# Kernel tuning notes

Hardware: AMD Instinct MI355X
Metric: run time of the kernel (lower is better)

## Reference

```python
import jax, jax.numpy as jnp
import numpy as np

N = 8192   # number of points (p) == number of reference points (r); must match for final bmm
D = 1024   # feature width of the Linear projections


def setup_inputs() -> dict:
    key = jax.random.key(0)
    ks = jax.random.split(key, 8)
    s = 1.0 / np.sqrt(D)
    return {
        "p": jax.random.normal(ks[0], (N, D), dtype=jnp.float32),
        "r": jax.random.normal(ks[1], (N, D), dtype=jnp.float32),
        "Wh": jax.random.uniform(ks[2], (D, D), jnp.float32, -s, s),
        "bh": jax.random.uniform(ks[3], (D,), jnp.float32, -s, s),
        "Wl": jax.random.uniform(ks[4], (D, D), jnp.float32, -s, s),
        "bl": jax.random.uniform(ks[5], (D,), jnp.float32, -s, s),
        "Wg": jax.random.uniform(ks[6], (D, D), jnp.float32, -s, s),
        "bg": jax.random.uniform(ks[7], (D,), jnp.float32, -s, s),
    }


def reference(p, r, Wh, bh, Wl, bl, Wg, bg):
    # Linear projections (torch Linear: x @ W.T + b)
    q = p @ Wh.T + bh          # [N, D]  M_h(p)
    k = r @ Wl.T + bl          # [N, D]  M_l(r)
    v = p @ Wg.T + bg          # [N, D]  M_g(p)
    scores = q @ k.T           # [N, N]  == bmm(q[None], k[None].transpose(1,2))[0]
    # torch softmax dim=1 on [1, N, N] normalizes over the QUERY axis -> axis=0 here
    attn = jax.nn.softmax(scores, axis=0)
    return p + attn @ v        # residual add
```

## Files before the change

### kernel.cpp

```cpp
#include <hip/hip_runtime.h>
#include <hip/hip_fp16.h>

typedef _Float16 f16;
typedef __attribute__((ext_vector_type(8))) _Float16 f16x8;
typedef __attribute__((ext_vector_type(4))) float f32x4;

#define NPTS 8192
#define DIM  1024
#define HL2E 0.721347520444482f
#define S2SHIFT 50.0f
#define TBUF (128 * 32)

__device__ __forceinline__ void glds16(const void* g, void* l) {
  __builtin_amdgcn_global_load_lds(
      (const __attribute__((address_space(1))) void*)g,
      (__attribute__((address_space(3))) void*)l, 16, 0, 0);
}

__global__ void cvt_f32_f16(const float* __restrict__ src, f16* __restrict__ dst, int n) {
  int i = (blockIdx.x * 256 + threadIdx.x) * 8;
  if (i >= n) return;
  const float4* s = (const float4*)(src + i);
  float4 a = s[0], b = s[1];
  f16x8 o;
  o[0] = (f16)a.x; o[1] = (f16)a.y; o[2] = (f16)a.z; o[3] = (f16)a.w;
  o[4] = (f16)b.x; o[5] = (f16)b.y; o[6] = (f16)b.z; o[7] = (f16)b.w;
  *(f16x8*)(dst + i) = o;
}

__global__ void zero_f32(float* __restrict__ p, int n) {
  int i = blockIdx.x * 256 + threadIdx.x;
  if (i < n) p[i] = 0.f;
}

__global__ void mk_scales(const float* __restrict__ colsum,
                          f16* __restrict__ ics2, f16* __restrict__ ics4) {
  int j = blockIdx.x * 256 + threadIdx.x;
  float r2 = rsqrtf(colsum[j]);
  ics2[j] = (f16)r2;
  ics4[j] = (f16)sqrtf(r2);
}

__global__ void vscale(f16* __restrict__ vt, const f16* __restrict__ ics2) {
  long i = ((long)blockIdx.x * 256 + threadIdx.x) * 8;
  f16x8 v = *(f16x8*)(vt + i);
  f16x8 s = *(const f16x8*)(ics2 + (i & (NPTS - 1)));
  *(f16x8*)(vt + i) = v * s;
}

template<int EPI, int SWZ>
__global__ __launch_bounds__(256, 2)
void gemm_bt(const f16* __restrict__ A, int lda,
             const f16* __restrict__ B, int ldb,
             int M, int N, int K,
             const float* __restrict__ bias,
             void* __restrict__ Cout, int ldc,
             const float* __restrict__ Res, int ldr,
             float* __restrict__ colsum, const f16* __restrict__ ics4) {
  __shared__ f16 sA[2 * TBUF];
  __shared__ f16 sB[2 * TBUF];
  const int t = threadIdx.x;
  const int w = t >> 6, l = t & 63;
  const int wm = (w >> 1) * 64, wn = (w & 1) * 64;
  long bi, bj;
  if (SWZ) {
    bi = (long)(blockIdx.x & 63) * 128;
    bj = (long)(blockIdx.x >> 6) * 128;
  } else {
    bi = (long)blockIdx.y * 128;
    bj = (long)blockIdx.x * 128;
  }
  const int lr = l & 15, lk = (l >> 4) * 8;

  const int grow = w * 16 + (l >> 2);
  const int gcol = (l & 3) * 8;
  const f16* gA = A + (bi + grow) * (long)lda + gcol;
  const f16* gB = B + (bj + grow) * (long)ldb + gcol;
  const int lw0 = (w * 16) * 32;
  const int lw1 = (64 + w * 16) * 32;

  const int sr = t >> 2, sc = (t & 3) * 8;
  const f16* gAs = A + (bi + sr) * (long)lda + sc;
  f16x8 ra0 = {}, ra1 = {}, icv = {};

  const int nk = K >> 5;

  if (EPI == 3) {
    ra0 = *(const f16x8*)gAs;
    ra1 = *(const f16x8*)(gAs + 64l * lda);
    icv = *(const f16x8*)(ics4 + sc);
    f16x8 t0 = ra0 * icv; t0 = t0 * t0;
    f16x8 t1 = ra1 * icv; t1 = t1 * t1;
    *(f16x8*)(sA + sr * 32 + sc) = t0;
    *(f16x8*)(sA + (sr + 64) * 32 + sc) = t1;
    if (nk > 1) {
      gAs += 32;
      ra0 = *(const f16x8*)gAs;
      ra1 = *(const f16x8*)(gAs + 64l * lda);
      icv = *(const f16x8*)(ics4 + 32 + sc);
    }
  } else {
    glds16(gA, sA + lw0);
    glds16(gA + 64l * lda, sA + lw1);
    gA += 32;
  }
  glds16(gB, sB + lw0);
  glds16(gB + 64l * ldb, sB + lw1);
  gB += 32;

  f32x4 acc[4][4] = {};

  for (int k = 0; k < nk; k++) {
    const int cur = (k & 1) * TBUF, nxt = TBUF - cur;
    __syncthreads();
    if (k + 1 < nk) {
      if (EPI == 3) {
        f16x8 t0 = ra0 * icv; t0 = t0 * t0;
        f16x8 t1 = ra1 * icv; t1 = t1 * t1;
        *(f16x8*)(sA + nxt + sr * 32 + sc) = t0;
        *(f16x8*)(sA + nxt + (sr + 64) * 32 + sc) = t1;
        if (k + 2 < nk) {
          gAs += 32;
          ra0 = *(const f16x8*)gAs;
          ra1 = *(const f16x8*)(gAs + 64l * lda);
          icv = *(const f16x8*)(ics4 + (k + 2) * 32 + sc);
        }
      } else {
        glds16(gA, sA + nxt + lw0);
        glds16(gA + 64l * lda, sA + nxt + lw1);
        gA += 32;
      }
      glds16(gB, sB + nxt + lw0);
      glds16(gB + 64l * ldb, sB + nxt + lw1);
      gB += 32;
    }
    f16x8 af[4], bf[4];
#pragma unroll
    for (int mt = 0; mt < 4; mt++)
      af[mt] = *(const f16x8*)(sA + cur + (wm + mt * 16 + lr) * 32 + lk);
#pragma unroll
    for (int nt = 0; nt < 4; nt++)
      bf[nt] = *(const f16x8*)(sB + cur + (wn + nt * 16 + lr) * 32 + lk);
#pragma unroll
    for (int mt = 0; mt < 4; mt++)
#pragma unroll
      for (int nt = 0; nt < 4; nt++)
        acc[mt][nt] = __builtin_amdgcn_mfma_f32_16x16x32_f16(af[mt], bf[nt], acc[mt][nt], 0, 0, 0);
  }

  const int rbase = (l >> 4) * 4;
#pragma unroll
  for (int nt = 0; nt < 4; nt++) {
    const long col = bj + wn + nt * 16 + lr;
    float csum = 0.f;
#pragma unroll
    for (int mt = 0; mt < 4; mt++) {
      const long row0 = bi + wm + mt * 16 + rbase;
      if (EPI == 0) {
        float bb = bias[col];
        f16* C = (f16*)Cout;
#pragma unroll
        for (int g = 0; g < 4; g++)
          C[(row0 + g) * ldc + col] = (f16)(acc[mt][nt][g] + bb);
      } else if (EPI == 1) {
        float bb = bias[col];
        union { unsigned long long u; f16 h[4]; } pk;
#pragma unroll
        for (int g = 0; g < 4; g++) pk.h[g] = (f16)(acc[mt][nt][g] + bb);
        *(unsigned long long*)((f16*)Cout + col * (long)ldc + row0) = pk.u;
      } else if (EPI == 3) {
        float* C = (float*)Cout;
#pragma unroll
        for (int g = 0; g < 4; g++)
          C[(row0 + g) * ldc + col] = acc[mt][nt][g] + Res[(row0 + g) * (long)ldr + col];
      } else {
        f16* C = (f16*)Cout;
#pragma unroll
        for (int g = 0; g < 4; g++) {
          float e = exp2f((acc[mt][nt][g] - S2SHIFT) * HL2E);
          e = fminf(e, 240.f);
          f16 eh = (f16)e;
          C[(row0 + g) * ldc + col] = eh;
          float ef = (float)eh;
          csum += ef * ef;
        }
      }
    }
    if (EPI == 4) {
      csum += __shfl_xor(csum, 16);
      csum += __shfl_xor(csum, 32);
      if (l < 16) atomicAdd(colsum + col, csum);
    }
  }
}

extern "C" void kernel_launch(void* const* d_in, const int* in_sizes, int n_in,
                              void* d_out, int out_size, void* d_ws, size_t ws_size,
                              hipStream_t stream) {
  const float* p  = (const float*)d_in[0];
  const float* r  = (const float*)d_in[1];
  const float* Wh = (const float*)d_in[2];
  const float* bh = (const float*)d_in[3];
  const float* Wl = (const float*)d_in[4];
  const float* bl = (const float*)d_in[5];
  const float* Wg = (const float*)d_in[6];
  const float* bg = (const float*)d_in[7];
  float* out = (float*)d_out;

  char* ws = (char*)d_ws;
  f16* q_h  = (f16*)(ws + (0ull  << 20));
  f16* k_h  = (f16*)(ws + (16ull << 20));
  f16* vt_h = (f16*)(ws + (32ull << 20));
  f16* p_h  = (f16*)(ws + (48ull << 20));
  f16* r_h  = (f16*)(ws + (64ull << 20));
  f16* wh_h = (f16*)(ws + (80ull << 20));
  f16* wl_h = (f16*)(ws + (82ull << 20));
  f16* wg_h = (f16*)(ws + (84ull << 20));
  f16* S    = (f16*)(ws + (96ull << 20));
  float* colsum = (float*)(ws + (224ull << 20));
  f16* ics2 = (f16*)(ws + (225ull << 20));
  f16* ics4 = (f16*)(ws + (226ull << 20));

  const int nP = NPTS * DIM, nW = DIM * DIM;
  cvt_f32_f16<<<nP / 2048, 256, 0, stream>>>(p,  p_h,  nP);
  cvt_f32_f16<<<nP / 2048, 256, 0, stream>>>(r,  r_h,  nP);
  cvt_f32_f16<<<nW / 2048, 256, 0, stream>>>(Wh, wh_h, nW);
  cvt_f32_f16<<<nW / 2048, 256, 0, stream>>>(Wl, wl_h, nW);
  cvt_f32_f16<<<nW / 2048, 256, 0, stream>>>(Wg, wg_h, nW);
  zero_f32<<<NPTS / 256, 256, 0, stream>>>(colsum, NPTS);

  dim3 blk(256);
  gemm_bt<0, 1><<<512, blk, 0, stream>>>(
      p_h, DIM, wh_h, DIM, NPTS, DIM, DIM, bh, q_h, DIM, nullptr, 0, nullptr, nullptr);
  gemm_bt<0, 1><<<512, blk, 0, stream>>>(
      r_h, DIM, wl_h, DIM, NPTS, DIM, DIM, bl, k_h, DIM, nullptr, 0, nullptr, nullptr);
  gemm_bt<1, 1><<<512, blk, 0, stream>>>(
      p_h, DIM, wg_h, DIM, NPTS, DIM, DIM, bg, vt_h, NPTS, nullptr, 0, nullptr, nullptr);
  gemm_bt<4, 0><<<dim3(NPTS / 128, NPTS / 128), blk, 0, stream>>>(
      q_h, DIM, k_h, DIM, NPTS, NPTS, DIM, nullptr, S, NPTS, nullptr, 0, colsum, nullptr);
  mk_scales<<<NPTS / 256, 256, 0, stream>>>(colsum, ics2, ics4);
  vscale<<<(NPTS / 8) * (DIM / 256), 256, 0, stream>>>(vt_h, ics2);
  gemm_bt<3, 1><<<512, blk, 0, stream>>>(
      S, NPTS, vt_h, NPTS, NPTS, DIM, NPTS, nullptr, out, DIM, p, DIM, colsum, ics4);
}
```

Measured before the change: 581.5 us.

## Split-K the attention-value GEMM with atomics and fuse the three projection launches

```diff
diff --git a/kernel.cpp b/kernel.cpp
--- a/kernel.cpp
+++ b/kernel.cpp
@@ -33,6 +33,11 @@
   if (i < n) p[i] = 0.f;
 }
 
+__global__ void init_out(const float* __restrict__ p, float* __restrict__ out) {
+  long i = ((long)blockIdx.x * 256 + threadIdx.x) * 4;
+  *(float4*)(out + i) = *(const float4*)(p + i);
+}
+
 __global__ void mk_scales(const float* __restrict__ colsum,
                           f16* __restrict__ ics2, f16* __restrict__ ics4) {
   int j = blockIdx.x * 256 + threadIdx.x;
@@ -48,90 +53,223 @@
   *(f16x8*)(vt + i) = v * s;
 }
 
-template<int EPI, int SWZ>
 __global__ __launch_bounds__(256, 2)
-void gemm_bt(const f16* __restrict__ A, int lda,
-             const f16* __restrict__ B, int ldb,
-             int M, int N, int K,
-             const float* __restrict__ bias,
-             void* __restrict__ Cout, int ldc,
-             const float* __restrict__ Res, int ldr,
-             float* __restrict__ colsum, const f16* __restrict__ ics4) {
+void proj_fused(const f16* __restrict__ p_h, const f16* __restrict__ r_h,
+                const f16* __restrict__ Wh, const f16* __restrict__ Wl,
+                const f16* __restrict__ Wg,
+                const float* __restrict__ bh, const float* __restrict__ bl,
+                const float* __restrict__ bg,
+                f16* __restrict__ q_h, f16* __restrict__ k_h,
+                f16* __restrict__ vt_h) {
   __shared__ f16 sA[2 * TBUF];
   __shared__ f16 sB[2 * TBUF];
+  const int sub = blockIdx.x >> 9;
+  const int bl_ = blockIdx.x & 511;
+  const long bi = (long)(bl_ & 63) * 128;
+  const long bj = (long)(bl_ >> 6) * 128;
+  const f16* A = (sub == 1) ? r_h : p_h;
+  const f16* B = (sub == 0) ? Wh : (sub == 1) ? Wl : Wg;
+  const float* bias = (sub == 0) ? bh : (sub == 1) ? bl : bg;
+
   const int t = threadIdx.x;
   const int w = t >> 6, l = t & 63;
   const int wm = (w >> 1) * 64, wn = (w & 1) * 64;
-  long bi, bj;
-  if (SWZ) {
-    bi = (long)(blockIdx.x & 63) * 128;
-    bj = (long)(blockIdx.x >> 6) * 128;
-  } else {
-    bi = (long)blockIdx.y * 128;
-    bj = (long)blockIdx.x * 128;
-  }
   const int lr = l & 15, lk = (l >> 4) * 8;
-
   const int grow = w * 16 + (l >> 2);
   const int gcol = (l & 3) * 8;
-  const f16* gA = A + (bi + grow) * (long)lda + gcol;
-  const f16* gB = B + (bj + grow) * (long)ldb + gcol;
-  const int lw0 = (w * 16) * 32;
-  const int lw1 = (64 + w * 16) * 32;
+  const f16* gA = A + (bi + grow) * (long)DIM + gcol;
+  const f16* gB = B + (bj + grow) * (long)DIM + gcol;
+  const int lw0 = (w * 16) * 32, lw1 = (64 + w * 16) * 32;
+
+  glds16(gA, sA + lw0);
+  glds16(gA + 64l * DIM, sA + lw1);
+  glds16(gB, sB + lw0);
+  glds16(gB + 64l * DIM, sB + lw1);
+  gA += 32; gB += 32;
+
+  f32x4 acc[4][4] = {};
+  const int nk = DIM / 32;
+  for (int k = 0; k < nk; k++) {
+    const int cur = (k & 1) * TBUF, nxt = TBUF - cur;
+    __syncthreads();
+    if (k + 1 < nk) {
+      glds16(gA, sA + nxt + lw0);
+      glds16(gA + 64l * DIM, sA + nxt + lw1);
+      glds16(gB, sB + nxt + lw0);
+      glds16(gB + 64l * DIM, sB + nxt + lw1);
+      gA += 32; gB += 32;
+    }
+    f16x8 af[4], bf[4];
+#pragma unroll
+    for (int mt = 0; mt < 4; mt++)
+      af[mt] = *(const f16x8*)(sA + cur + (wm + mt * 16 + lr) * 32 + lk);
+#pragma unroll
+    for (int nt = 0; nt < 4; nt++)
+      bf[nt] = *(const f16x8*)(sB + cur + (wn + nt * 16 + lr) * 32 + lk);
+#pragma unroll
+    for (int mt = 0; mt < 4; mt++)
+#pragma unroll
+      for (int nt = 0; nt < 4; nt++)
+        acc[mt][nt] = __builtin_amdgcn_mfma_f32_16x16x32_f16(af[mt], bf[nt], acc[mt][nt], 0, 0, 0);
+  }
+
+  const int rbase = (l >> 4) * 4;
+  f16* C = (sub == 0) ? q_h : (sub == 1) ? k_h : vt_h;
+#pragma unroll
+  for (int nt = 0; nt < 4; nt++) {
+    const long col = bj + wn + nt * 16 + lr;
+    const float bb = bias[col];
+#pragma unroll
+    for (int mt = 0; mt < 4; mt++) {
+      const long row0 = bi + wm + mt * 16 + rbase;
+      if (sub < 2) {
+#pragma unroll
+        for (int g = 0; g < 4; g++)
+          C[(row0 + g) * DIM + col] = (f16)(acc[mt][nt][g] + bb);
+      } else {
+        union { unsigned long long u; f16 h[4]; } pk;
+#pragma unroll
+        for (int g = 0; g < 4; g++) pk.h[g] = (f16)(acc[mt][nt][g] + bb);
+        *(unsigned long long*)(C + col * (long)NPTS + row0) = pk.u;
+      }
+    }
+  }
+}
+
+__global__ __launch_bounds__(256, 2)
+void gemm_qk(const f16* __restrict__ A, const f16* __restrict__ B,
+             f16* __restrict__ S, float* __restrict__ colsum) {
+  __shared__ f16 sA[2 * TBUF];
+  __shared__ f16 sB[2 * TBUF];
+  const long bi = (long)blockIdx.y * 128;
+  const long bj = (long)blockIdx.x * 128;
+  const int t = threadIdx.x;
+  const int w = t >> 6, l = t & 63;
+  const int wm = (w >> 1) * 64, wn = (w & 1) * 64;
+  const int lr = l & 15, lk = (l >> 4) * 8;
+  const int grow = w * 16 + (l >> 2);
+  const int gcol = (l & 3) * 8;
+  const f16* gA = A + (bi + grow) * (long)DIM + gcol;
+  const f16* gB = B + (bj + grow) * (long)DIM + gcol;
+  const int lw0 = (w * 16) * 32, lw1 = (64 + w * 16) * 32;
+
+  glds16(gA, sA + lw0);
+  glds16(gA + 64l * DIM, sA + lw1);
+  glds16(gB, sB + lw0);
+  glds16(gB + 64l * DIM, sB + lw1);
+  gA += 32; gB += 32;
+
+  f32x4 acc[4][4] = {};
+  const int nk = DIM / 32;
+  for (int k = 0; k < nk; k++) {
+    const int cur = (k & 1) * TBUF, nxt = TBUF - cur;
+    __syncthreads();
+    if (k + 1 < nk) {
+      glds16(gA, sA + nxt + lw0);
+      glds16(gA + 64l * DIM, sA + nxt + lw1);
+      glds16(gB, sB + nxt + lw0);
+      glds16(gB + 64l * DIM, sB + nxt + lw1);
+      gA += 32; gB += 32;
+    }
+    f16x8 af[4], bf[4];
+#pragma unroll
+    for (int mt = 0; mt < 4; mt++)
+      af[mt] = *(const f16x8*)(sA + cur + (wm + mt * 16 + lr) * 32 + lk);
+#pragma unroll
+    for (int nt = 0; nt < 4; nt++)
+      bf[nt] = *(const f16x8*)(sB + cur + (wn + nt * 16 + lr) * 32 + lk);
+#pragma unroll
+    for (int mt = 0; mt < 4; mt++)
+#pragma unroll
+      for (int nt = 0; nt < 4; nt++)
+        acc[mt][nt] = __builtin_amdgcn_mfma_f32_16x16x32_f16(af[mt], bf[nt], acc[mt][nt], 0, 0, 0);
+  }
+
+  const int rbase = (l >> 4) * 4;
+#pragma unroll
+  for (int nt = 0; nt < 4; nt++) {
+    const long col = bj + wn + nt * 16 + lr;
+    float csum = 0.f;
+#pragma unroll
+    for (int mt = 0; mt < 4; mt++) {
+      const long row0 = bi + wm + mt * 16 + rbase;
+#pragma unroll
+      for (int g = 0; g < 4; g++) {
+        float e = exp2f((acc[mt][nt][g] - S2SHIFT) * HL2E);
+        e = fminf(e, 240.f);
+        f16 eh = (f16)e;
+        S[(row0 + g) * NPTS + col] = eh;
+        float ef = (float)eh;
+        csum += ef * ef;
+      }
+    }
+    csum += __shfl_xor(csum, 16);
+    csum += __shfl_xor(csum, 32);
+    if (l < 16) atomicAdd(colsum + col, csum);
+  }
+}
+
+__global__ __launch_bounds__(256, 2)
+void gemm_pv(const f16* __restrict__ Sm, const f16* __restrict__ vt,
+             const f16* __restrict__ ics4, float* __restrict__ out) {
+  __shared__ f16 sA[2 * TBUF];
+  __shared__ f16 sB[2 * TBUF];
+  const int split = blockIdx.x >> 9;
+  const int bl_ = blockIdx.x & 511;
+  const long bi = (long)(bl_ & 63) * 128;
+  const long bj = (long)(bl_ >> 6) * 128;
+  const long koff = (long)split * 2048;
+
+  const int t = threadIdx.x;
+  const int w = t >> 6, l = t & 63;
+  const int wm = (w >> 1) * 64, wn = (w & 1) * 64;
+  const int lr = l & 15, lk = (l >> 4) * 8;
+  const int grow = w * 16 + (l >> 2);
+  const int gcol = (l & 3) * 8;
+  const f16* gB = vt + (bj + grow) * (long)NPTS + koff + gcol;
+  const int lw0 = (w * 16) * 32, lw1 = (64 + w * 16) * 32;
 
   const int sr = t >> 2, sc = (t & 3) * 8;
-  const f16* gAs = A + (bi + sr) * (long)lda + sc;
-  f16x8 ra0 = {}, ra1 = {}, icv = {};
-
-  const int nk = K >> 5;
-
-  if (EPI == 3) {
-    ra0 = *(const f16x8*)gAs;
-    ra1 = *(const f16x8*)(gAs + 64l * lda);
-    icv = *(const f16x8*)(ics4 + sc);
+  const f16* gAs = Sm + (bi + sr) * (long)NPTS + koff + sc;
+  const f16* gIc = ics4 + koff + sc;
+  f16x8 ra0, ra1, icv;
+
+  const int nk = 2048 / 32;
+
+  ra0 = *(const f16x8*)gAs;
+  ra1 = *(const f16x8*)(gAs + 64l * NPTS);
+  icv = *(const f16x8*)gIc;
+  {
     f16x8 t0 = ra0 * icv; t0 = t0 * t0;
     f16x8 t1 = ra1 * icv; t1 = t1 * t1;
     *(f16x8*)(sA + sr * 32 + sc) = t0;
     *(f16x8*)(sA + (sr + 64) * 32 + sc) = t1;
-    if (nk > 1) {
-      gAs += 32;
-      ra0 = *(const f16x8*)gAs;
-      ra1 = *(const f16x8*)(gAs + 64l * lda);
-      icv = *(const f16x8*)(ics4 + 32 + sc);
-    }
-  } else {
-    glds16(gA, sA + lw0);
-    glds16(gA + 64l * lda, sA + lw1);
-    gA += 32;
-  }
+  }
+  gAs += 32; gIc += 32;
+  ra0 = *(const f16x8*)gAs;
+  ra1 = *(const f16x8*)(gAs + 64l * NPTS);
+  icv = *(const f16x8*)gIc;
   glds16(gB, sB + lw0);
-  glds16(gB + 64l * ldb, sB + lw1);
+  glds16(gB + 64l * NPTS, sB + lw1);
   gB += 32;
 
   f32x4 acc[4][4] = {};
-
   for (int k = 0; k < nk; k++) {
     const int cur = (k & 1) * TBUF, nxt = TBUF - cur;
     __syncthreads();
     if (k + 1 < nk) {
-      if (EPI == 3) {
-        f16x8 t0 = ra0 * icv; t0 = t0 * t0;
-        f16x8 t1 = ra1 * icv; t1 = t1 * t1;
-        *(f16x8*)(sA + nxt + sr * 32 + sc) = t0;
-        *(f16x8*)(sA + nxt + (sr + 64) * 32 + sc) = t1;
-        if (k + 2 < nk) {
-          gAs += 32;
-          ra0 = *(const f16x8*)gAs;
-          ra1 = *(const f16x8*)(gAs + 64l * lda);
-          icv = *(const f16x8*)(ics4 + (k + 2) * 32 + sc);
-        }
-      } else {
-        glds16(gA, sA + nxt + lw0);
-        glds16(gA + 64l * lda, sA + nxt + lw1);
-        gA += 32;
+      f16x8 t0 = ra0 * icv; t0 = t0 * t0;
+      f16x8 t1 = ra1 * icv; t1 = t1 * t1;
+      *(f16x8*)(sA + nxt + sr * 32 + sc) = t0;
+      *(f16x8*)(sA + nxt + (sr + 64) * 32 + sc) = t1;
+      if (k + 2 < nk) {
+        gAs += 32; gIc += 32;
+        ra0 = *(const f16x8*)gAs;
+        ra1 = *(const f16x8*)(gAs + 64l * NPTS);
+        icv = *(const f16x8*)gIc;
       }
       glds16(gB, sB + nxt + lw0);
-      glds16(gB + 64l * ldb, sB + nxt + lw1);
+      glds16(gB + 64l * NPTS, sB + nxt + lw1);
       gB += 32;
     }
     f16x8 af[4], bf[4];
@@ -152,44 +290,12 @@
 #pragma unroll
   for (int nt = 0; nt < 4; nt++) {
     const long col = bj + wn + nt * 16 + lr;
-    float csum = 0.f;
 #pragma unroll
     for (int mt = 0; mt < 4; mt++) {
       const long row0 = bi + wm + mt * 16 + rbase;
-      if (EPI == 0) {
-        float bb = bias[col];
-        f16* C = (f16*)Cout;
-#pragma unroll
-        for (int g = 0; g < 4; g++)
-          C[(row0 + g) * ldc + col] = (f16)(acc[mt][nt][g] + bb);
-      } else if (EPI == 1) {
-        float bb = bias[col];
-        union { unsigned long long u; f16 h[4]; } pk;
-#pragma unroll
-        for (int g = 0; g < 4; g++) pk.h[g] = (f16)(acc[mt][nt][g] + bb);
-        *(unsigned long long*)((f16*)Cout + col * (long)ldc + row0) = pk.u;
-      } else if (EPI == 3) {
-        float* C = (float*)Cout;
-#pragma unroll
-        for (int g = 0; g < 4; g++)
-          C[(row0 + g) * ldc + col] = acc[mt][nt][g] + Res[(row0 + g) * (long)ldr + col];
-      } else {
-        f16* C = (f16*)Cout;
-#pragma unroll
-        for (int g = 0; g < 4; g++) {
-          float e = exp2f((acc[mt][nt][g] - S2SHIFT) * HL2E);
-          e = fminf(e, 240.f);
-          f16 eh = (f16)e;
-          C[(row0 + g) * ldc + col] = eh;
-          float ef = (float)eh;
-          csum += ef * ef;
-        }
-      }
-    }
-    if (EPI == 4) {
-      csum += __shfl_xor(csum, 16);
-      csum += __shfl_xor(csum, 32);
-      if (l < 16) atomicAdd(colsum + col, csum);
+#pragma unroll
+      for (int g = 0; g < 4; g++)
+        atomicAdd(out + (row0 + g) * DIM + col, acc[mt][nt][g]);
     }
   }
 }
@@ -228,18 +334,13 @@
   cvt_f32_f16<<<nW / 2048, 256, 0, stream>>>(Wl, wl_h, nW);
   cvt_f32_f16<<<nW / 2048, 256, 0, stream>>>(Wg, wg_h, nW);
   zero_f32<<<NPTS / 256, 256, 0, stream>>>(colsum, NPTS);
+  init_out<<<nP / 1024, 256, 0, stream>>>(p, out);
 
   dim3 blk(256);
-  gemm_bt<0, 1><<<512, blk, 0, stream>>>(
-      p_h, DIM, wh_h, DIM, NPTS, DIM, DIM, bh, q_h, DIM, nullptr, 0, nullptr, nullptr);
-  gemm_bt<0, 1><<<512, blk, 0, stream>>>(
-      r_h, DIM, wl_h, DIM, NPTS, DIM, DIM, bl, k_h, DIM, nullptr, 0, nullptr, nullptr);
-  gemm_bt<1, 1><<<512, blk, 0, stream>>>(
-      p_h, DIM, wg_h, DIM, NPTS, DIM, DIM, bg, vt_h, NPTS, nullptr, 0, nullptr, nullptr);
-  gemm_bt<4, 0><<<dim3(NPTS / 128, NPTS / 128), blk, 0, stream>>>(
-      q_h, DIM, k_h, DIM, NPTS, NPTS, DIM, nullptr, S, NPTS, nullptr, 0, colsum, nullptr);
+  proj_fused<<<1536, blk, 0, stream>>>(p_h, r_h, wh_h, wl_h, wg_h,
+                                       bh, bl, bg, q_h, k_h, vt_h);
+  gemm_qk<<<dim3(64, 64), blk, 0, stream>>>(q_h, k_h, S, colsum);
   mk_scales<<<NPTS / 256, 256, 0, stream>>>(colsum, ics2, ics4);
   vscale<<<(NPTS / 8) * (DIM / 256), 256, 0, stream>>>(vt_h, ics2);
-  gemm_bt<3, 1><<<512, blk, 0, stream>>>(
-      S, NPTS, vt_h, NPTS, NPTS, DIM, NPTS, nullptr, out, DIM, p, DIM, colsum, ics4);
-}
+  gemm_pv<<<2048, blk, 0, stream>>>(S, vt_h, ics4, out);
+}
```

Measured after the change: 616.1 us. +6.0%, slower.
